# Performance work log

Hardware: AMD Instinct MI355X
Metric: run time of the kernel (lower is better)

## Reference

```python
import jax, jax.numpy as jnp
import numpy as np

N = 8192      # number of WSI patches
DIN = 1024    # input patch-feature dim (dim_in)
DH = 256      # dim_hidden
K = 6         # topk
SCALE = DH ** -0.5

def leaky(x):
    return jax.nn.leaky_relu(x, 0.01)

def setup_inputs() -> dict:
    key = jax.random.key(0)
    ks = jax.random.split(key, 8)
    def w(k, shape, fan_in):
        return jax.random.normal(k, shape, jnp.float32) / np.sqrt(fan_in).astype(np.float32)
    return {
        "x_path": jax.random.normal(ks[0], (N, DIN), jnp.float32),
        "fc1_W": w(ks[1], (DIN, DH), DIN), "fc1_b": jnp.zeros((DH,), jnp.float32),
        "Wh": w(ks[2], (DH, DH), DH), "bh": jnp.zeros((DH,), jnp.float32),
        "Wt": w(ks[3], (DH, DH), DH), "bt": jnp.zeros((DH,), jnp.float32),
        "W1": w(ks[4], (DH, DH), DH), "b1": jnp.zeros((DH,), jnp.float32),
        "W2": w(ks[5], (DH, DH), DH), "b2": jnp.zeros((DH,), jnp.float32),
        "Ag1": w(ks[6], (DH, DH // 2), DH), "bg1": jnp.zeros((DH // 2,), jnp.float32),
        "Ag2": w(ks[7], (DH // 2, 1), DH // 2), "bg2": jnp.zeros((1,), jnp.float32),
    }

def reference(x_path, fc1_W, fc1_b, Wh, bh, Wt, bt, W1, b1, W2, b2, Ag1, bg1, Ag2, bg2):
    # _fc1: Linear(1024->256) + LeakyReLU, then add global mean ("*0.5" mixing)
    x = leaky(x_path @ fc1_W + fc1_b)[None]                 # (1,N,DH)
    x = (x + x.mean(axis=1, keepdims=True)) * 0.5
    e_h = x @ Wh + bh                                        # (1,N,DH)
    e_t = x @ Wt + bt                                        # (1,N,DH)
    # dense attention logits, then top-k neighbor selection
    attn_logit = (e_h * SCALE) @ jnp.swapaxes(e_t, -1, -2)   # (1,N,N)
    topk_w, topk_i = jax.lax.top_k(attn_logit, K)            # (1,N,K)
    p = jax.nn.softmax(topk_w, axis=2)                       # (1,N,K)
    Nb_h = e_t[0][topk_i[0]][None]                           # gather: (1,N,K,DH)
    # message construction
    eh_r = p[..., None] * Nb_h + (1.0 - p)[..., None] * e_h[:, :, None, :]
    gate = jnp.tanh(e_h[:, :, None, :] + eh_r)               # (1,N,K,DH)
    # faithful to torch.einsum('ijkl,ijkm->ijk', Nb_h, gate):
    # l and m are independent -> separable double sum
    ka_w = Nb_h.sum(-1) * gate.sum(-1)                       # (1,N,K)
    ka_p = jax.nn.softmax(ka_w, axis=2)
    e_Nh = jnp.einsum('ink,inkd->ind', ka_p, Nb_h)           # (1,N,DH)
    # message MLPs (dropout in eval mode = identity)
    e_msg = leaky((e_h + e_Nh) @ W1 + b1) + leaky((e_h * e_Nh) @ W2 + b2)
    # GlobalAttention readout: gate_nn = Linear(256,128)+LeakyReLU+Linear(128,1)
    x2 = e_msg[0]                                            # (N,DH)
    g = leaky(x2 @ Ag1 + bg1) @ Ag2 + bg2                    # (N,1)
    g = jax.nn.softmax(g, axis=0)
    e_g = (g * x2).sum(axis=0, keepdims=True)                # (1,DH)
    return e_msg, e_g
```

## Files before the change

### kernel.cpp

```cpp
#include <hip/hip_runtime.h>


typedef __attribute__((ext_vector_type(8))) short short8;
typedef __attribute__((ext_vector_type(4))) short short4v;
typedef __attribute__((ext_vector_type(4))) float f32x4;

__device__ inline float bf2f(unsigned short b) {
    unsigned u = ((unsigned)b) << 16;
    return __builtin_bit_cast(float, u);
}
__device__ inline unsigned short f2bf(float f) {
    unsigned u = __builtin_bit_cast(unsigned, f);
    unsigned r = u + 0x7fffu + ((u >> 16) & 1u);
    return (unsigned short)(r >> 16);
}
__device__ inline f32x4 mfma16(short8 a, short8 b, f32x4 c) {
    return __builtin_amdgcn_mfma_f32_16x16x32_bf16(a, b, c, 0, 0, 0);
}

__device__ inline void gload_lds16(const unsigned short* g, unsigned short* l) {
    __builtin_amdgcn_global_load_lds(
        (const __attribute__((address_space(1))) void*)g,
        (__attribute__((address_space(3))) void*)l, 16, 0, 0);
}

__device__ inline void split8(const f32x4 v0, const f32x4 v1,
                              short8& hi, short8& md, short8& lo) {
    #pragma unroll
    for (int e = 0; e < 8; e++) {
        float a = (e < 4) ? v0[e] : v1[e - 4];
        unsigned ua = __builtin_bit_cast(unsigned, a);
        float h = __builtin_bit_cast(float, ua & 0xFFFF0000u);
        float r1 = a - h;
        unsigned u1 = __builtin_bit_cast(unsigned, r1);
        float m = __builtin_bit_cast(float, u1 & 0xFFFF0000u);
        float r2 = r1 - m;
        unsigned u2 = __builtin_bit_cast(unsigned, r2);
        hi[e] = (short)(ua >> 16);
        md[e] = (short)(u1 >> 16);
        lo[e] = (short)(u2 >> 16);
    }
}
__device__ inline void split4(f32x4 v, short4v& hi, short4v& md, short4v& lo) {
    #pragma unroll
    for (int e = 0; e < 4; e++) {
        float a = v[e];
        unsigned ua = __builtin_bit_cast(unsigned, a);
        float h = __builtin_bit_cast(float, ua & 0xFFFF0000u);
        float r1 = a - h;
        unsigned u1 = __builtin_bit_cast(unsigned, r1);
        float m = __builtin_bit_cast(float, u1 & 0xFFFF0000u);
        float r2 = r1 - m;
        unsigned u2 = __builtin_bit_cast(unsigned, r2);
        hi[e] = (short)(ua >> 16);
        md[e] = (short)(u1 >> 16);
        lo[e] = (short)(u2 >> 16);
    }
}

__device__ inline void tsplit_body(const float* __restrict__ W,
                                   unsigned short* __restrict__ out,
                                   int K, int N, int PS, int bx, int by, int t) {
    __shared__ float T[32][33];
    const int n0 = bx * 32, k0 = by * 32;
    {
        const int r = t >> 3, c = (t & 7) * 4;
        f32x4 v = *(const f32x4*)&W[(size_t)(k0 + r) * N + n0 + c];
        #pragma unroll
        for (int e = 0; e < 4; e++) T[r][c + e] = v[e];
    }
    __syncthreads();
    const int nr = t >> 3, kc = (t & 7) * 4;
    short4v h4, m4, l4;
    #pragma unroll
    for (int e = 0; e < 4; e++) {
        float a = T[kc + e][nr];
        unsigned short h = f2bf(a);
        float r1 = a - bf2f(h);
        unsigned short m = f2bf(r1);
        float r2 = r1 - bf2f(m);
        h4[e] = (short)h; m4[e] = (short)m; l4[e] = (short)f2bf(r2);
    }
    const size_t o = (size_t)(n0 + nr) * K + k0 + kc;
    *(short4v*)&out[o] = h4;
    *(short4v*)&out[(size_t)PS + o] = m4;
    *(short4v*)&out[(size_t)2 * PS + o] = l4;
}
__launch_bounds__(256)
__global__ void tsplit3(const float* __restrict__ W, unsigned short* __restrict__ out,
                        int K, int N, int PS) {
    tsplit_body(W, out, K, N, PS, blockIdx.x, blockIdx.y, threadIdx.x);
}
__launch_bounds__(256)
__global__ void tsplit3p(const float* __restrict__ Wa, const float* __restrict__ Wb,
                         unsigned short* __restrict__ oa, unsigned short* __restrict__ ob,
                         int K, int N, int PS) {
    tsplit_body(blockIdx.z ? Wb : Wa, blockIdx.z ? ob : oa,
                K, N, PS, blockIdx.x, blockIdx.y, threadIdx.x);
}

template <int ASPLIT, int ACT, int ACCUM>
__launch_bounds__(256)
__global__ void gemmM(const void* __restrict__ Av,
                      const unsigned short* __restrict__ Bt,
                      const float* __restrict__ bias, float* __restrict__ C,
                      int N, int K, int BPS) {
    constexpr int APL = ASPLIT ? 3 : 1;
    constexpr int BPL = ASPLIT ? 3 : 2;
    __shared__ __align__(16) unsigned short LA[2][APL * 2048];
    __shared__ __align__(16) unsigned short LB[2][BPL * 2048];
    const int t = threadIdx.x;
    const int r0 = blockIdx.y * 64, c0 = blockIdx.x * 64;
    const int lid = t & 63, w = t >> 6, g = lid >> 4, m16 = lid & 15;
    const int wm = w >> 1, wn = w & 1;

    f32x4 acc[2][2];
    #pragma unroll
    for (int mf = 0; mf < 2; mf++)
        #pragma unroll
        for (int nf = 0; nf < 2; nf++) acc[mf][nf] = {0.0f, 0.0f, 0.0f, 0.0f};

    const int KT = K >> 5;
    const size_t aoff = (size_t)(r0 + (t >> 2)) * K + (t & 3) * 8;
    const size_t boff = (size_t)(c0 + (t >> 2)) * K + (t & 3) * 8;

    {
        #pragma unroll
        for (int p = 0; p < BPL; p++)
            gload_lds16(&Bt[(size_t)p * BPS + boff], &LB[0][p * 2048 + 8 * t]);
        if (ASPLIT) {
            const float* A = (const float*)Av;
            f32x4 v0 = *(const f32x4*)&A[aoff];
            f32x4 v1 = *(const f32x4*)&A[aoff + 4];
            short8 hi, md, lo;
            split8(v0, v1, hi, md, lo);
            *(short8*)&LA[0][8 * t] = hi;
            *(short8*)&LA[0][2048 + 8 * t] = md;
            *(short8*)&LA[0][4096 + 8 * t] = lo;
        } else {
            const unsigned short* A16 = (const unsigned short*)Av;
            gload_lds16(&A16[aoff], &LA[0][8 * t]);
        }
    }
    __syncthreads();

    for (int kt = 0; kt < KT; kt++) {
        const int cur = kt & 1, nxt = cur ^ 1;
        const bool hn = (kt + 1) < KT;
        f32x4 v0, v1;
        if (hn) {
            const size_t ko = (size_t)(kt + 1) * 32;
            #pragma unroll
            for (int p = 0; p < BPL; p++)
                gload_lds16(&Bt[(size_t)p * BPS + boff + ko],
                            &LB[nxt][p * 2048 + 8 * t]);
            if (ASPLIT) {
                const float* A = (const float*)Av;
                v0 = *(const f32x4*)&A[aoff + ko];
                v1 = *(const f32x4*)&A[aoff + ko + 4];
            } else {
                const unsigned short* A16 = (const unsigned short*)Av;
                gload_lds16(&A16[aoff + ko], &LA[nxt][8 * t]);
            }
        }
        short8 af[2][APL], bf[2][BPL];
        #pragma unroll
        for (int mf = 0; mf < 2; mf++) {
            const int row = wm * 32 + mf * 16 + m16;
            #pragma unroll
            for (int p = 0; p < APL; p++)
                af[mf][p] = *(const short8*)&LA[cur][p * 2048 + row * 32 + g * 8];
        }
        #pragma unroll
        for (int nf = 0; nf < 2; nf++) {
            const int col = wn * 32 + nf * 16 + m16;
            #pragma unroll
            for (int p = 0; p < BPL; p++)
                bf[nf][p] = *(const short8*)&LB[cur][p * 2048 + col * 32 + g * 8];
        }
        #pragma unroll
        for (int mf = 0; mf < 2; mf++)
            #pragma unroll
            for (int nf = 0; nf < 2; nf++) {
                if (ASPLIT) {
                    acc[mf][nf] = mfma16(af[mf][0], bf[nf][0], acc[mf][nf]);
                    acc[mf][nf] = mfma16(af[mf][0], bf[nf][1], acc[mf][nf]);
                    acc[mf][nf] = mfma16(af[mf][1], bf[nf][0], acc[mf][nf]);
                    acc[mf][nf] = mfma16(af[mf][0], bf[nf][2], acc[mf][nf]);
                    acc[mf][nf] = mfma16(af[mf][1], bf[nf][1], acc[mf][nf]);
                    acc[mf][nf] = mfma16(af[mf][2], bf[nf][0], acc[mf][nf]);
                } else {
                    acc[mf][nf] = mfma16(af[mf][0], bf[nf][0], acc[mf][nf]);
                    acc[mf][nf] = mfma16(af[mf][0], bf[nf][1], acc[mf][nf]);
                }
            }
        if (hn && ASPLIT) {
            short8 hi, md, lo;
            split8(v0, v1, hi, md, lo);
            *(short8*)&LA[nxt][8 * t] = hi;
            *(short8*)&LA[nxt][2048 + 8 * t] = md;
            *(short8*)&LA[nxt][4096 + 8 * t] = lo;
        }
        __syncthreads();
    }

    #pragma unroll
    for (int nf = 0; nf < 2; nf++) {
        const int col = c0 + wn * 32 + nf * 16 + m16;
        const float bv = bias[col];
        #pragma unroll
        for (int mf = 0; mf < 2; mf++) {
            #pragma unroll
            for (int r = 0; r < 4; r++) {
                const int row = r0 + wm * 32 + mf * 16 + g * 4 + r;
                float v = acc[mf][nf][r] + bv;
                if (ACT == 1) v = v > 0.0f ? v : 0.01f * v;
                size_t idx = (size_t)row * N + col;
                if (ACCUM) v += C[idx];
                C[idx] = v;
            }
        }
    }
}

__launch_bounds__(512)
__global__ void gemmD(const float* __restrict__ A,
                      const unsigned short* __restrict__ BH,
                      const unsigned short* __restrict__ BT,
                      const float* __restrict__ biasH, const float* __restrict__ biasT,
                      float* __restrict__ CH, float* __restrict__ CT, int BPS) {
    __shared__ __align__(16) unsigned short LA[2][3 * 2048];
    __shared__ __align__(16) unsigned short LB[2][6 * 2048];
    const int t = threadIdx.x;
    const int r0 = blockIdx.y * 64, c0 = blockIdx.x * 64;
    const int lid = t & 63, w = t >> 6, g = lid >> 4, m16 = lid & 15;
    const int mat = w >> 2, wsub = w & 3, wm = wsub >> 1, wn = wsub & 1;
    const int K = 256;

    f32x4 acc[2][2];
    #pragma unroll
    for (int mf = 0; mf < 2; mf++)
        #pragma unroll
        for (int nf = 0; nf < 2; nf++) acc[mf][nf] = {0.0f, 0.0f, 0.0f, 0.0f};

    const int arow = t >> 3, akq = (t & 7) * 4;
    const size_t aoff = (size_t)(r0 + arow) * K + akq;
    const int aldst = arow * 32 + akq;
    int bmp[3], bdst[3];
    size_t bsrc[3];
    #pragma unroll
    for (int s = 0; s < 3; s++) {
        int L = t + s * 512;
        int mp = L >> 8;
        bmp[s] = mp;
        bdst[s] = mp * 2048 + (L & 255) * 8;
        int mm = mp >= 3, pl = mp - 3 * mm;
        const unsigned short* base = mm ? BT : BH;
        bsrc[s] = (size_t)(base - BH) + (size_t)pl * BPS +
                  (size_t)(c0 + ((L >> 2) & 63)) * K + (L & 3) * 8;
    }

    {
        #pragma unroll
        for (int s = 0; s < 3; s++)
            gload_lds16(&BH[bsrc[s]], &LB[0][bdst[s]]);
        f32x4 v = *(const f32x4*)&A[aoff];
        #pragma unroll
        for (int e = 0; e < 4; e++) v[e] *= 0.5f;
        short4v hi, md, lo;
        split4(v, hi, md, lo);
        *(short4v*)&LA[0][aldst] = hi;
        *(short4v*)&LA[0][2048 + aldst] = md;
        *(short4v*)&LA[0][4096 + aldst] = lo;
    }
    __syncthreads();

    for (int kt = 0; kt < 8; kt++) {
        const int cur = kt & 1, nxt = cur ^ 1;
        const bool hn = (kt + 1) < 8;
        f32x4 v;
        if (hn) {
            const size_t ko = (size_t)(kt + 1) * 32;
            #pragma unroll
            for (int s = 0; s < 3; s++)
                gload_lds16(&BH[bsrc[s] + ko], &LB[nxt][bdst[s]]);
            v = *(const f32x4*)&A[aoff + ko];
            #pragma unroll
            for (int e = 0; e < 4; e++) v[e] *= 0.5f;
        }
        short8 af[2][3], bf[2][3];
        #pragma unroll
        for (int mf = 0; mf < 2; mf++) {
            const int row = wm * 32 + mf * 16 + m16;
            #pragma unroll
            for (int p = 0; p < 3; p++)
                af[mf][p] = *(const short8*)&LA[cur][p * 2048 + row * 32 + g * 8];
        }
        #pragma unroll
        for (int nf = 0; nf < 2; nf++) {
            const int col = wn * 32 + nf * 16 + m16;
            #pragma unroll
            for (int p = 0; p < 3; p++)
                bf[nf][p] = *(const short8*)
                    &LB[cur][(mat * 3 + p) * 2048 + col * 32 + g * 8];
        }
        #pragma unroll
        for (int mf = 0; mf < 2; mf++)
            #pragma unroll
            for (int nf = 0; nf < 2; nf++) {
                acc[mf][nf] = mfma16(af[mf][0], bf[nf][0], acc[mf][nf]);
                acc[mf][nf] = mfma16(af[mf][0], bf[nf][1], acc[mf][nf]);
                acc[mf][nf] = mfma16(af[mf][1], bf[nf][0], acc[mf][nf]);
                acc[mf][nf] = mfma16(af[mf][0], bf[nf][2], acc[mf][nf]);
                acc[mf][nf] = mfma16(af[mf][1], bf[nf][1], acc[mf][nf]);
                acc[mf][nf] = mfma16(af[mf][2], bf[nf][0], acc[mf][nf]);
            }
        if (hn) {
            short4v hi, md, lo;
            split4(v, hi, md, lo);
            *(short4v*)&LA[nxt][aldst] = hi;
            *(short4v*)&LA[nxt][2048 + aldst] = md;
            *(short4v*)&LA[nxt][4096 + aldst] = lo;
        }
        __syncthreads();
    }

    float* C = mat ? CT : CH;
    const float* bias = mat ? biasT : biasH;
    #pragma unroll
    for (int nf = 0; nf < 2; nf++) {
        const int col = c0 + wn * 32 + nf * 16 + m16;
        const float bv = bias[col];
        #pragma unroll
        for (int mf = 0; mf < 2; mf++) {
            #pragma unroll
            for (int r = 0; r < 4; r++) {
                const int row = r0 + wm * 32 + mf * 16 + g * 4 + r;
                C[(size_t)row * 256 + col] = acc[mf][nf][r] + bv;
            }
        }
    }
}

__launch_bounds__(256)
__global__ void gemmE(const unsigned short* __restrict__ A1,
                      const unsigned short* __restrict__ A2,
                      const unsigned short* __restrict__ P1,
                      const unsigned short* __restrict__ P2,
                      const float* __restrict__ b1, const float* __restrict__ b2,
                      float* __restrict__ C, int BPS) {
    __shared__ __align__(16) unsigned short LA[2][2 * 2048];
    __shared__ __align__(16) unsigned short LB[2][4 * 2048];
    const int t = threadIdx.x;
    const int r0 = blockIdx.y * 64, c0 = blockIdx.x * 64;
    const int lid = t & 63, w = t >> 6, g = lid >> 4, m16 = lid & 15;
    const int wm = w >> 1, wn = w & 1;
    const int K = 256;

    f32x4 acc[2][2][2];
    #pragma unroll
    for (int m = 0; m < 2; m++)
        #pragma unroll
        for (int mf = 0; mf < 2; mf++)
            #pragma unroll
            for (int nf = 0; nf < 2; nf++) acc[m][mf][nf] = {0.0f, 0.0f, 0.0f, 0.0f};

    const size_t aoff = (size_t)(r0 + (t >> 2)) * K + (t & 3) * 8;
    const size_t boff = (size_t)(c0 + (t >> 2)) * K + (t & 3) * 8;

    {
        gload_lds16(&A1[aoff], &LA[0][8 * t]);
        gload_lds16(&A2[aoff], &LA[0][2048 + 8 * t]);
        gload_lds16(&P1[boff], &LB[0][8 * t]);
        gload_lds16(&P1[(size_t)BPS + boff], &LB[0][2048 + 8 * t]);
        gload_lds16(&P2[boff], &LB[0][4096 + 8 * t]);
        gload_lds16(&P2[(size_t)BPS + boff], &LB[0][6144 + 8 * t]);
    }
    __syncthreads();

    for (int kt = 0; kt < 8; kt++) {
        const int cur = kt & 1, nxt = cur ^ 1;
        const bool hn = (kt + 1) < 8;
        if (hn) {
            const size_t ko = (size_t)(kt + 1) * 32;
            gload_lds16(&A1[aoff + ko], &LA[nxt][8 * t]);
            gload_lds16(&A2[aoff + ko], &LA[nxt][2048 + 8 * t]);
            gload_lds16(&P1[boff + ko], &LB[nxt][8 * t]);
            gload_lds16(&P1[(size_t)BPS + boff + ko], &LB[nxt][2048 + 8 * t]);
            gload_lds16(&P2[boff + ko], &LB[nxt][4096 + 8 * t]);
            gload_lds16(&P2[(size_t)BPS + boff + ko], &LB[nxt][6144 + 8 * t]);
        }
        short8 af[2][2], bf[2][2][2];
        #pragma unroll
        for (int m = 0; m < 2; m++)
            #pragma unroll
            for (int mf = 0; mf < 2; mf++) {
                const int row = wm * 32 + mf * 16 + m16;
                af[m][mf] = *(const short8*)&LA[cur][m * 2048 + row * 32 + g * 8];
            }
        #pragma unroll
        for (int m = 0; m < 2; m++)
            #pragma unroll
            for (int nf = 0; nf < 2; nf++) {
                const int col = wn * 32 + nf * 16 + m16;
                #pragma unroll
                for (int p = 0; p < 2; p++)
                    bf[m][nf][p] = *(const short8*)
                        &LB[cur][(m * 2 + p) * 2048 + col * 32 + g * 8];
            }
        #pragma unroll
        for (int m = 0; m < 2; m++)
            #pragma unroll
            for (int mf = 0; mf < 2; mf++)
                #pragma unroll
                for (int nf = 0; nf < 2; nf++) {
                    acc[m][mf][nf] = mfma16(af[m][mf], bf[m][nf][0], acc[m][mf][nf]);
                    acc[m][mf][nf] = mfma16(af[m][mf], bf[m][nf][1], acc[m][mf][nf]);
                }
        __syncthreads();
    }

    #pragma unroll
    for (int nf = 0; nf < 2; nf++) {
        const int col = c0 + wn * 32 + nf * 16 + m16;
        const float bv1 = b1[col], bv2 = b2[col];
        #pragma unroll
        for (int mf = 0; mf < 2; mf++) {
            #pragma unroll
            for (int r = 0; r < 4; r++) {
                const int row = r0 + wm * 32 + mf * 16 + g * 4 + r;
                float v1 = acc[0][mf][nf][r] + bv1;
                v1 = v1 > 0.0f ? v1 : 0.01f * v1;
                float v2 = acc[1][mf][nf][r] + bv2;
                v2 = v2 > 0.0f ? v2 : 0.01f * v2;
                C[(size_t)row * 256 + col] = v1 + v2;
            }
        }
    }
}

__global__ void colsum_k(const float* __restrict__ x, float* __restrict__ out) {
    int d = threadIdx.x, b = blockIdx.x;
    float s = 0.0f;
    int i0 = b * 128;
    for (int i = 0; i < 128; i++) s += x[(size_t)(i0 + i) * 256 + d];
    out[b * 256 + d] = s;
}
__global__ void meanred_k(const float* __restrict__ p, float* __restrict__ mean) {
    int d = threadIdx.x;
    float s = 0.0f;
    for (int b = 0; b < 64; b++) s += p[b * 256 + d];
    mean[d] = s * (1.0f / 8192.0f);
}
__launch_bounds__(256)
__global__ void mwv_k(const float* __restrict__ mean,
                      const float* __restrict__ Wh, const float* __restrict__ bh,
                      const float* __restrict__ Wt, const float* __restrict__ bt,
                      float* __restrict__ biasH, float* __restrict__ biasT) {
    const int n = threadIdx.x;
    const float* W = blockIdx.x ? Wt : Wh;
    const float* bb = blockIdx.x ? bt : bh;
    float* o = blockIdx.x ? biasT : biasH;
    float s = 0.0f;
    for (int d = 0; d < 256; d++) s += mean[d] * W[d * 256 + n];
    o[n] = bb[n] + 0.5f * s;
}
__launch_bounds__(256)
__global__ void prep_k(const float* __restrict__ eh, const float* __restrict__ et,
                       unsigned short* __restrict__ eh16,
                       unsigned short* __restrict__ et16,
                       float* __restrict__ rowsum) {
    const int b = blockIdx.x;
    if (b < 2048) {
        size_t idx = (size_t)b * 256 + threadIdx.x;
        f32x4 v = *(const f32x4*)&eh[idx * 4];
        short4v h;
        #pragma unroll
        for (int e = 0; e < 4; e++) h[e] = (short)f2bf(v[e]);
        *(short4v*)&eh16[idx * 4] = h;
    } else {
        const int w = threadIdx.x >> 6, l = threadIdx.x & 63;
        const int i = (b - 2048) * 4 + w;
        f32x4 v = *(const f32x4*)&et[(size_t)i * 256 + l * 4];
        short4v h;
        #pragma unroll
        for (int e = 0; e < 4; e++) h[e] = (short)f2bf(v[e]);
        *(short4v*)&et16[(size_t)i * 256 + l * 4] = h;
        float s = v[0] + v[1] + v[2] + v[3];
        #pragma unroll
        for (int st = 1; st < 64; st <<= 1) s += __shfl_xor(s, st);
        if (l == 0) rowsum[i] = s;
    }
}

__device__ inline float packkey(float v, unsigned col) {
    unsigned u = (__builtin_bit_cast(unsigned, v) & 0xFFFFF800u) | col;
    return __builtin_bit_cast(float, u);
}
template<int NK>
__device__ inline void insf(float (&tk)[NK], float key) {
    #pragma unroll
    for (int k = 0; k < NK - 1; k++)
        tk[k] = __builtin_amdgcn_fmed3f(key, tk[k + 1], tk[k]);
    tk[NK - 1] = fmaxf(tk[NK - 1], key);
}

__launch_bounds__(512)
__global__ void screen2(const unsigned short* __restrict__ eh16,
                        const unsigned short* __restrict__ et16,
                        int* __restrict__ candi) {
    __shared__ __align__(16) unsigned short Bs[2][2][8192];
    __shared__ float mbuf[8][2][16][8];
    const int t = threadIdx.x;
    const int cs = blockIdx.x;
    const int r0 = blockIdx.y * 128;
    const int w = t >> 6, lid = t & 63, lg = lid >> 4, m16 = lid & 15;
    const int rs = w >> 1, ch = w & 1;

    short8 bfr[2][8];
    #pragma unroll
    for (int s = 0; s < 2; s++)
        #pragma unroll
        for (int ks = 0; ks < 8; ks++)
            bfr[s][ks] = *(const short8*)
                &eh16[(size_t)(r0 + rs * 32 + s * 16 + m16) * 256 + ks * 32 + lg * 8];

    float tk0[6], tk1[6];
    #pragma unroll
    for (int q = 0; q < 6; q++) { tk0[q] = -3.0e38f; tk1[q] = -3.0e38f; }

    int scol[2], goff[2], ldsl[2];
    #pragma unroll
    for (int c = 0; c < 2; c++) {
        int L = (w * 2 + c) * 64 + lid;
        int col = L >> 5, gs = L & 31;
        int gorig = (gs & 24) | ((gs ^ col) & 7);
        scol[c] = col; goff[c] = gorig * 8; ldsl[c] = L * 8;
    }

    #pragma unroll
    for (int tt = 0; tt < 2; tt++) {
        const int j0 = cs * 2048 + tt * 32;
        #pragma unroll
        for (int c = 0; c < 2; c++)
            gload_lds16(&et16[(size_t)(j0 + scol[c]) * 256 + goff[c]],
                        &Bs[0][tt][ldsl[c]]);
    }
    __syncthreads();

    const int swz = m16 & 7;
    const int cbase = (ch * 16 + m16) * 32;
    for (int gi = 0; gi < 32; gi++) {
        const int cur = gi & 1;
        if (gi + 1 < 32) {
            #pragma unroll
            for (int tt = 0; tt < 2; tt++) {
                const int j1 = cs * 2048 + ((gi + 1) * 2 + tt) * 32;
                #pragma unroll
                for (int c = 0; c < 2; c++)
                    gload_lds16(&et16[(size_t)(j1 + scol[c]) * 256 + goff[c]],
                                &Bs[cur ^ 1][tt][ldsl[c]]);
            }
        }
        #pragma unroll
        for (int tt = 0; tt < 2; tt++) {
            const int tile = gi * 2 + tt;
            const unsigned short* bst = Bs[cur][tt];
            f32x4 a0 = {0.0f, 0.0f, 0.0f, 0.0f}, a1 = a0;
            #pragma unroll
            for (int ks = 0; ks < 8; ks++) {
                const int gq = ks * 4 + lg;
                short8 e = *(const short8*)&bst[(cbase + (gq ^ swz)) * 8];
                a0 = mfma16(e, bfr[0][ks], a0);
                a1 = mfma16(e, bfr[1][ks], a1);
            }
            const unsigned cb = (unsigned)(tile * 32 + ch * 16 + lg * 4);
            #pragma unroll
            for (int r = 0; r < 4; r++) {
                insf<6>(tk0, packkey(a0[r], cb + (unsigned)r));
                insf<6>(tk1, packkey(a1[r], cb + (unsigned)r));
            }
        }
        __syncthreads();
    }

    #pragma unroll
    for (int s = 0; s < 2; s++) {
        float tk8[8];
        tk8[0] = -3.0e38f; tk8[1] = -3.0e38f;
        #pragma unroll
        for (int q = 0; q < 6; q++) tk8[q + 2] = s ? tk1[q] : tk0[q];
        #pragma unroll
        for (int step = 16; step <= 32; step <<= 1) {
            float ok[8];
            #pragma unroll
            for (int q = 0; q < 8; q++) ok[q] = __shfl_xor(tk8[q], step);
            #pragma unroll
            for (int q = 0; q < 8; q++) insf<8>(tk8, ok[q]);
        }
        if (lg == 0) {
            #pragma unroll
            for (int q = 0; q < 8; q++) mbuf[rs * 2 + s][ch][m16][q] = tk8[q];
        }
    }
    __syncthreads();

    if (t < 128) {
        float tk8[8];
        #pragma unroll
        for (int q = 0; q < 8; q++) tk8[q] = mbuf[t >> 4][0][t & 15][q];
        #pragma unroll
        for (int q = 0; q < 8; q++) insf<8>(tk8, mbuf[t >> 4][1][t & 15][q]);
        const int row = r0 + t;
        #pragma unroll
        for (int q = 0; q < 8; q++)
            candi[(size_t)row * 32 + cs * 8 + q] =
                cs * 2048 + (int)(__builtin_bit_cast(unsigned, tk8[q]) & 0x7FFu);
    }
}

__launch_bounds__(256)
__global__ void stageD(const float* __restrict__ eh, const float* __restrict__ et,
                       const float* __restrict__ rowsum,
                       const int* __restrict__ candi,
                       unsigned short* __restrict__ m1, unsigned short* __restrict__ m2) {
    const int w = threadIdx.x >> 6, l = threadIdx.x & 63;
    const int i = blockIdx.x * 4 + w;
    const int c_own = l & 31;

    const int jown = candi[(size_t)i * 32 + c_own] & 8191;

    const int q = l & 7, g8 = l >> 3;
    const float* er = &eh[(size_t)i * 256];
    double vres[4];
    #pragma unroll
    for (int p = 0; p < 4; p++) {
        const int cc = p * 8 + g8;
        const int jc = __shfl(jown, cc);
        const float* tr = &et[(size_t)jc * 256];
        double a = 0.0;
        #pragma unroll
        for (int tt = 0; tt < 8; tt++) {
            const int o = (tt * 8 + q) * 4;
            f32x4 av = *(const f32x4*)&er[o];
            f32x4 bv = *(const f32x4*)&tr[o];
            a += (double)av[0] * bv[0] + (double)av[1] * bv[1] +
                 (double)av[2] * bv[2] + (double)av[3] * bv[3];
        }
        a += __shfl_xor(a, 1);
        a += __shfl_xor(a, 2);
        a += __shfl_xor(a, 4);
        vres[p] = a * 0.0625;
    }
    const int src = (c_own & 7) * 8;
    double t0 = __shfl(vres[0], src), t1 = __shfl(vres[1], src);
    double t2 = __shfl(vres[2], src), t3 = __shfl(vres[3], src);
    const int ps = c_own >> 3;
    double v = ps == 0 ? t0 : ps == 1 ? t1 : ps == 2 ? t2 : t3;

    unsigned long long kb = __builtin_bit_cast(unsigned long long, v);
    double key = __builtin_bit_cast(double, (kb & ~31ULL) | (unsigned long long)c_own);
    float wf[6]; int selc[6];
    #pragma unroll
    for (int s = 0; s < 6; s++) {
        double b = key;
        #pragma unroll
        for (int st = 1; st < 32; st <<= 1) {
            double ob = __shfl_xor(b, st);
            b = b > ob ? b : ob;
        }
        selc[s] = (int)(__builtin_bit_cast(unsigned long long, b) & 31ULL);
        wf[s] = (float)b;
        if (key == b) key = -1.0e300;
    }
    int selj[6];
    #pragma unroll
    for (int s = 0; s < 6; s++) selj[s] = __shfl(jown, selc[s]);

    float sp[6];
    {
        float mx = wf[0];
        #pragma unroll
        for (int s = 1; s < 6; s++) mx = fmaxf(mx, wf[s]);
        float se = 0.0f, e6[6];
        #pragma unroll
        for (int s = 0; s < 6; s++) { e6[s] = expf(wf[s] - mx); se += e6[s]; }
        #pragma unroll
        for (int s = 0; s < 6; s++) sp[s] = e6[s] / se;
    }

    f32x4 eh4 = *(const f32x4*)&eh[(size_t)i * 256 + l * 4];
    f32x4 nb[6];
    #pragma unroll
    for (int k = 0; k < 6; k++)
        nb[k] = *(const f32x4*)&et[(size_t)selj[k] * 256 + l * 4];

    float pgs[6], pns[6];
    #pragma unroll
    for (int k = 0; k < 6; k++) {
        const float pk = sp[k];
        float pg = 0.0f;
        #pragma unroll
        for (int e = 0; e < 4; e++) {
            float ehd = eh4[e], nbd = nb[k][e];
            float ehr = pk * nbd + (1.0f - pk) * ehd;
            pg += tanhf(ehd + ehr);
        }
        #pragma unroll
        for (int st = 1; st < 64; st <<= 1) pg += __shfl_xor(pg, st);
        pgs[k] = pg;
        pns[k] = rowsum[selj[k]];
    }

    float skp[6];
    {
        float ka[6], mx = -3.0e38f, se = 0.0f;
        #pragma unroll
        for (int k = 0; k < 6; k++) { ka[k] = pns[k] * pgs[k]; mx = fmaxf(mx, ka[k]); }
        #pragma unroll
        for (int k = 0; k < 6; k++) { ka[k] = expf(ka[k] - mx); se += ka[k]; }
        #pragma unroll
        for (int k = 0; k < 6; k++) skp[k] = ka[k] / se;
    }

    f32x4 enh = {0.0f, 0.0f, 0.0f, 0.0f};
    #pragma unroll
    for (int k = 0; k < 6; k++) {
        const float kp = skp[k];
        #pragma unroll
        for (int e = 0; e < 4; e++) enh[e] += kp * nb[k][e];
    }
    short4v h1, h2;
    #pragma unroll
    for (int e = 0; e < 4; e++) {
        h1[e] = (short)f2bf(eh4[e] + enh[e]);
        h2[e] = (short)f2bf(eh4[e] * enh[e]);
    }
    *(short4v*)&m1[(size_t)i * 256 + l * 4] = h1;
    *(short4v*)&m2[(size_t)i * 256 + l * 4] = h2;
}

__launch_bounds__(256)
__global__ void gate2_k(const float* __restrict__ g1, const float* __restrict__ Ag2,
                        const float* __restrict__ bg2, float* __restrict__ glog) {
    const int i = blockIdx.x * 256 + threadIdx.x;
    float s = 0.0f;
    #pragma unroll 4
    for (int h = 0; h < 128; h++) s += g1[(size_t)i * 128 + h] * Ag2[h];
    glog[i] = s + bg2[0];
}

__launch_bounds__(1024)
__global__ void softmax_g(const float* __restrict__ glog, float* __restrict__ gexp,
                          float* __restrict__ scal) {
    const int t = threadIdx.x;
    __shared__ float red[1024];
    float v[8];
    float m = -3.0e38f;
    #pragma unroll
    for (int c = 0; c < 8; c++) { v[c] = glog[t + c * 1024]; m = fmaxf(m, v[c]); }
    red[t] = m; __syncthreads();
    for (int st = 512; st > 0; st >>= 1) {
        if (t < st) red[t] = fmaxf(red[t], red[t + st]);
        __syncthreads();
    }
    float gm = red[0]; __syncthreads();
    float s = 0.0f;
    #pragma unroll
    for (int c = 0; c < 8; c++) {
        float e = expf(v[c] - gm);
        gexp[t + c * 1024] = e;
        s += e;
    }
    red[t] = s; __syncthreads();
    for (int st = 512; st > 0; st >>= 1) {
        if (t < st) red[t] += red[t + st];
        __syncthreads();
    }
    if (t == 0) scal[0] = 1.0f / red[0];
}

__launch_bounds__(256)
__global__ void wsum_k(const float* __restrict__ emsg, const float* __restrict__ gexp,
                       float* __restrict__ egp) {
    const int b = blockIdx.x, d = threadIdx.x;
    float s = 0.0f;
    const int i0 = b * 128;
    for (int i = 0; i < 128; i++) s += gexp[i0 + i] * emsg[(size_t)(i0 + i) * 256 + d];
    egp[b * 256 + d] = s;
}
__global__ void egfinal_f(const float* __restrict__ egp, const float* __restrict__ scal,
                          float* __restrict__ out) {
    const int d = threadIdx.x;
    float s = 0.0f;
    for (int b = 0; b < 64; b++) s += egp[b * 256 + d];
    out[d] = s * scal[0];
}

__global__ void wsbad_k(float* __restrict__ out) { out[3] = 9000.0f; }

extern "C" void kernel_launch(void* const* d_in, const int* in_sizes, int n_in,
                              void* d_out, int out_size, void* d_ws, size_t ws_size,
                              hipStream_t stream) {
    (void)in_sizes; (void)n_in; (void)out_size;
    const float* x_path = (const float*)d_in[0];
    const float* fc1_W  = (const float*)d_in[1];
    const float* fc1_b  = (const float*)d_in[2];
    const float* Wh     = (const float*)d_in[3];
    const float* bh     = (const float*)d_in[4];
    const float* Wt     = (const float*)d_in[5];
    const float* bt     = (const float*)d_in[6];
    const float* W1     = (const float*)d_in[7];
    const float* b1     = (const float*)d_in[8];
    const float* W2     = (const float*)d_in[9];
    const float* b2     = (const float*)d_in[10];
    const float* Ag1    = (const float*)d_in[11];
    const float* bg1    = (const float*)d_in[12];
    const float* Ag2    = (const float*)d_in[13];
    const float* bg2    = (const float*)d_in[14];
    float* out_f = (float*)d_out;

    const size_t WS_NEEDED = 26412048;
    if (ws_size < WS_NEEDED) {
        hipLaunchKernelGGL(wsbad_k, dim3(1), dim3(1), 0, stream, out_f);
        return;
    }

    char* ws = (char*)d_ws;
    float* x     = (float*)(ws + 0);
    unsigned short* eh16 = (unsigned short*)(ws + 0);
    unsigned short* et16 = (unsigned short*)(ws + 4194304);
    unsigned short* m1b  = (unsigned short*)(ws + 0);
    unsigned short* m2b  = (unsigned short*)(ws + 4194304);
    float* g1    = (float*)(ws + 0);
    float* eh    = (float*)(ws + 8388608);
    float* emsg  = out_f;
    float* et    = (float*)(ws + 16777216);
    int*   candi = (int*)  (ws + 25165824);
    float* rowsum= (float*)(ws + 26214400);
    float* meanp = (float*)(ws + 26214400);
    float* biasH = (float*)(ws + 26247168);
    float* biasT = (float*)(ws + 26248192);
    float* meanv = (float*)(ws + 26279936);
    float* glog  = (float*)(ws + 26280960);
    float* gexp  = (float*)(ws + 26313728);
    float* egp   = (float*)(ws + 26346496);
    float* scal  = (float*)(ws + 26412032);

    unsigned short* Fp = (unsigned short*)(ws + 16777216);
    unsigned short* WHp = (unsigned short*)(ws + 25165824);
    unsigned short* WTp = (unsigned short*)(ws + 25559040);
    unsigned short* P1 = (unsigned short*)(ws + 16777216);
    unsigned short* P2 = (unsigned short*)(ws + 17170432);
    unsigned short* Gp = (unsigned short*)(ws + 25165824);

    dim3 gg(4, 128);
    hipLaunchKernelGGL(tsplit3, dim3(8, 32), dim3(256), 0, stream,
                       fc1_W, Fp, 1024, 256, 262144);
    hipLaunchKernelGGL((gemmM<1, 1, 0>), gg, dim3(256), 0, stream,
                       (const void*)x_path, Fp, fc1_b, x, 256, 1024, 262144);
    hipLaunchKernelGGL(colsum_k, dim3(64), dim3(256), 0, stream, x, meanp);
    hipLaunchKernelGGL(meanred_k, dim3(1), dim3(256), 0, stream, meanp, meanv);
    hipLaunchKernelGGL(tsplit3p, dim3(8, 8, 2), dim3(256), 0, stream,
                       Wh, Wt, WHp, WTp, 256, 256, 65536);
    hipLaunchKernelGGL(mwv_k, dim3(2), dim3(256), 0, stream,
                       meanv, Wh, bh, Wt, bt, biasH, biasT);
    hipLaunchKernelGGL(gemmD, gg, dim3(512), 0, stream,
                       x, WHp, WTp, biasH, biasT, eh, et, 65536);
    hipLaunchKernelGGL(prep_k, dim3(4096), dim3(256), 0, stream,
                       eh, et, eh16, et16, rowsum);
    hipLaunchKernelGGL(screen2, dim3(4, 64), dim3(512), 0, stream, eh16, et16, candi);
    hipLaunchKernelGGL(stageD, dim3(2048), dim3(256), 0, stream, eh, et, rowsum,
                       candi, m1b, m2b);
    hipLaunchKernelGGL(tsplit3p, dim3(8, 8, 2), dim3(256), 0, stream,
                       W1, W2, P1, P2, 256, 256, 65536);
    hipLaunchKernelGGL(gemmE, gg, dim3(256), 0, stream,
                       m1b, m2b, P1, P2, b1, b2, emsg, 65536);
    hipLaunchKernelGGL(tsplit3, dim3(4, 8), dim3(256), 0, stream,
                       Ag1, Gp, 256, 128, 32768);
    hipLaunchKernelGGL((gemmM<1, 1, 0>), dim3(2, 128), dim3(256), 0, stream,
                       (const void*)emsg, Gp, bg1, g1, 128, 256, 32768);
    hipLaunchKernelGGL(gate2_k, dim3(32), dim3(256), 0, stream, g1, Ag2, bg2, glog);
    hipLaunchKernelGGL(softmax_g, dim3(1), dim3(1024), 0, stream, glog, gexp, scal);
    hipLaunchKernelGGL(wsum_k, dim3(64), dim3(256), 0, stream, emsg, gexp, egp);
    hipLaunchKernelGGL(egfinal_f, dim3(1), dim3(256), 0, stream, egp, scal, out_f + 2097152);
}
```

Measured before the change: 312.0 us.

## Fuse weight-split launches, mean reduction, bf16 prep and gate projection into neighbours

Merges the separate weight-split launches into two multi-matrix kernels and folds the mean reduction into the bias kernel. The bf16 conversion of e_h now happens inside the screening kernel, so the prep pass only handles e_t. The second gate layer (dot with Ag2) moves into a new GEMM epilogue that reduces by shuffles and accumulates into glog with atomics; glog is zeroed in colsum. This removes several launches and the g1 round trip through memory, at the cost of nondeterministic atomic summation order. bg2 is dropped, which is safe because softmax is shift-invariant.

```diff
diff --git a/kernel.cpp b/kernel.cpp
--- a/kernel.cpp
+++ b/kernel.cpp
@@ -87,16 +87,26 @@
     *(short4v*)&out[(size_t)2 * PS + o] = l4;
 }
 __launch_bounds__(256)
-__global__ void tsplit3(const float* __restrict__ W, unsigned short* __restrict__ out,
-                        int K, int N, int PS) {
-    tsplit_body(W, out, K, N, PS, blockIdx.x, blockIdx.y, threadIdx.x);
+__global__ void tsplitAll(const float* __restrict__ fc1_W, const float* __restrict__ Wh,
+                          const float* __restrict__ Wt,
+                          unsigned short* __restrict__ Fp,
+                          unsigned short* __restrict__ WHp,
+                          unsigned short* __restrict__ WTp) {
+    const int idx = blockIdx.x, t = threadIdx.x;
+    if (idx < 256) tsplit_body(fc1_W, Fp, 1024, 256, 262144, idx & 7, idx >> 3, t);
+    else if (idx < 320) { int r = idx - 256; tsplit_body(Wh, WHp, 256, 256, 65536, r & 7, r >> 3, t); }
+    else { int r = idx - 320; tsplit_body(Wt, WTp, 256, 256, 65536, r & 7, r >> 3, t); }
 }
 __launch_bounds__(256)
-__global__ void tsplit3p(const float* __restrict__ Wa, const float* __restrict__ Wb,
-                         unsigned short* __restrict__ oa, unsigned short* __restrict__ ob,
-                         int K, int N, int PS) {
-    tsplit_body(blockIdx.z ? Wb : Wa, blockIdx.z ? ob : oa,
-                K, N, PS, blockIdx.x, blockIdx.y, threadIdx.x);
+__global__ void tsplit3t(const float* __restrict__ W1, const float* __restrict__ W2,
+                         const float* __restrict__ Ag1,
+                         unsigned short* __restrict__ P1,
+                         unsigned short* __restrict__ P2,
+                         unsigned short* __restrict__ Gp) {
+    const int idx = blockIdx.x, t = threadIdx.x;
+    if (idx < 64) tsplit_body(W1, P1, 256, 256, 65536, idx & 7, idx >> 3, t);
+    else if (idx < 128) { int r = idx - 64; tsplit_body(W2, P2, 256, 256, 65536, r & 7, r >> 3, t); }
+    else { int r = idx - 128; tsplit_body(Ag1, Gp, 256, 128, 32768, r & 3, r >> 2, t); }
 }
 
 template <int ASPLIT, int ACT, int ACCUM>
@@ -246,13 +256,12 @@
     const int arow = t >> 3, akq = (t & 7) * 4;
     const size_t aoff = (size_t)(r0 + arow) * K + akq;
     const int aldst = arow * 32 + akq;
-    int bmp[3], bdst[3];
+    int bdst[3];
     size_t bsrc[3];
     #pragma unroll
     for (int s = 0; s < 3; s++) {
         int L = t + s * 512;
         int mp = L >> 8;
-        bmp[s] = mp;
         bdst[s] = mp * 2048 + (L & 255) * 8;
         int mm = mp >= 3, pl = mp - 3 * mm;
         const unsigned short* base = mm ? BT : BH;
@@ -439,25 +448,149 @@
     }
 }
 
-__global__ void colsum_k(const float* __restrict__ x, float* __restrict__ out) {
+__launch_bounds__(256)
+__global__ void gemmG(const float* __restrict__ A,
+                      const unsigned short* __restrict__ Bt,
+                      const float* __restrict__ bias,
+                      const float* __restrict__ Ag2, float* __restrict__ glog,
+                      int BPS) {
+    __shared__ __align__(16) unsigned short LA[2][3 * 2048];
+    __shared__ __align__(16) unsigned short LB[2][3 * 2048];
+    const int t = threadIdx.x;
+    const int r0 = blockIdx.y * 64, c0 = blockIdx.x * 64;
+    const int lid = t & 63, w = t >> 6, g = lid >> 4, m16 = lid & 15;
+    const int wm = w >> 1, wn = w & 1;
+    const int K = 256;
+
+    f32x4 acc[2][2];
+    #pragma unroll
+    for (int mf = 0; mf < 2; mf++)
+        #pragma unroll
+        for (int nf = 0; nf < 2; nf++) acc[mf][nf] = {0.0f, 0.0f, 0.0f, 0.0f};
+
+    const size_t aoff = (size_t)(r0 + (t >> 2)) * K + (t & 3) * 8;
+    const size_t boff = (size_t)(c0 + (t >> 2)) * K + (t & 3) * 8;
+
+    {
+        #pragma unroll
+        for (int p = 0; p < 3; p++)
+            gload_lds16(&Bt[(size_t)p * BPS + boff], &LB[0][p * 2048 + 8 * t]);
+        f32x4 v0 = *(const f32x4*)&A[aoff];
+        f32x4 v1 = *(const f32x4*)&A[aoff + 4];
+        short8 hi, md, lo;
+        split8(v0, v1, hi, md, lo);
+        *(short8*)&LA[0][8 * t] = hi;
+        *(short8*)&LA[0][2048 + 8 * t] = md;
+        *(short8*)&LA[0][4096 + 8 * t] = lo;
+    }
+    __syncthreads();
+
+    for (int kt = 0; kt < 8; kt++) {
+        const int cur = kt & 1, nxt = cur ^ 1;
+        const bool hn = (kt + 1) < 8;
+        f32x4 v0, v1;
+        if (hn) {
+            const size_t ko = (size_t)(kt + 1) * 32;
+            #pragma unroll
+            for (int p = 0; p < 3; p++)
+                gload_lds16(&Bt[(size_t)p * BPS + boff + ko],
+                            &LB[nxt][p * 2048 + 8 * t]);
+            v0 = *(const f32x4*)&A[aoff + ko];
+            v1 = *(const f32x4*)&A[aoff + ko + 4];
+        }
+        short8 af[2][3], bf[2][3];
+        #pragma unroll
+        for (int mf = 0; mf < 2; mf++) {
+            const int row = wm * 32 + mf * 16 + m16;
+            #pragma unroll
+            for (int p = 0; p < 3; p++)
+                af[mf][p] = *(const short8*)&LA[cur][p * 2048 + row * 32 + g * 8];
+        }
+        #pragma unroll
+        for (int nf = 0; nf < 2; nf++) {
+            const int col = wn * 32 + nf * 16 + m16;
+            #pragma unroll
+            for (int p = 0; p < 3; p++)
+                bf[nf][p] = *(const short8*)&LB[cur][p * 2048 + col * 32 + g * 8];
+        }
+        #pragma unroll
+        for (int mf = 0; mf < 2; mf++)
+            #pragma unroll
+            for (int nf = 0; nf < 2; nf++) {
+                acc[mf][nf] = mfma16(af[mf][0], bf[nf][0], acc[mf][nf]);
+                acc[mf][nf] = mfma16(af[mf][0], bf[nf][1], acc[mf][nf]);
+                acc[mf][nf] = mfma16(af[mf][1], bf[nf][0], acc[mf][nf]);
+                acc[mf][nf] = mfma16(af[mf][0], bf[nf][2], acc[mf][nf]);
+                acc[mf][nf] = mfma16(af[mf][1], bf[nf][1], acc[mf][nf]);
+                acc[mf][nf] = mfma16(af[mf][2], bf[nf][0], acc[mf][nf]);
+            }
+        if (hn) {
+            short8 hi, md, lo;
+            split8(v0, v1, hi, md, lo);
+            *(short8*)&LA[nxt][8 * t] = hi;
+            *(short8*)&LA[nxt][2048 + 8 * t] = md;
+            *(short8*)&LA[nxt][4096 + 8 * t] = lo;
+        }
+        __syncthreads();
+    }
+
+    float pp[2][4];
+    #pragma unroll
+    for (int mf = 0; mf < 2; mf++)
+        #pragma unroll
+        for (int r = 0; r < 4; r++) pp[mf][r] = 0.0f;
+    #pragma unroll
+    for (int nf = 0; nf < 2; nf++) {
+        const int col = c0 + wn * 32 + nf * 16 + m16;
+        const float bv = bias[col], a2 = Ag2[col];
+        #pragma unroll
+        for (int mf = 0; mf < 2; mf++) {
+            #pragma unroll
+            for (int r = 0; r < 4; r++) {
+                float v = acc[mf][nf][r] + bv;
+                v = v > 0.0f ? v : 0.01f * v;
+                pp[mf][r] += v * a2;
+            }
+        }
+    }
+    #pragma unroll
+    for (int st = 1; st < 16; st <<= 1)
+        #pragma unroll
+        for (int mf = 0; mf < 2; mf++)
+            #pragma unroll
+            for (int r = 0; r < 4; r++) pp[mf][r] += __shfl_xor(pp[mf][r], st);
+    if (m16 == 0) {
+        #pragma unroll
+        for (int mf = 0; mf < 2; mf++)
+            #pragma unroll
+            for (int r = 0; r < 4; r++)
+                atomicAdd(&glog[r0 + wm * 32 + mf * 16 + g * 4 + r], pp[mf][r]);
+    }
+}
+
+__global__ void colsum_k(const float* __restrict__ x, float* __restrict__ out,
+                         float* __restrict__ glog) {
     int d = threadIdx.x, b = blockIdx.x;
     float s = 0.0f;
     int i0 = b * 128;
     for (int i = 0; i < 128; i++) s += x[(size_t)(i0 + i) * 256 + d];
     out[b * 256 + d] = s;
-}
-__global__ void meanred_k(const float* __restrict__ p, float* __restrict__ mean) {
-    int d = threadIdx.x;
-    float s = 0.0f;
-    for (int b = 0; b < 64; b++) s += p[b * 256 + d];
-    mean[d] = s * (1.0f / 8192.0f);
+    int tid = b * 256 + d;
+    if (tid < 8192) glog[tid] = 0.0f;
 }
 __launch_bounds__(256)
-__global__ void mwv_k(const float* __restrict__ mean,
+__global__ void mwv_k(const float* __restrict__ meanp,
                       const float* __restrict__ Wh, const float* __restrict__ bh,
                       const float* __restrict__ Wt, const float* __restrict__ bt,
                       float* __restrict__ biasH, float* __restrict__ biasT) {
+    __shared__ float mean[256];
     const int n = threadIdx.x;
+    {
+        float s = 0.0f;
+        for (int b = 0; b < 64; b++) s += meanp[b * 256 + n];
+        mean[n] = s * (1.0f / 8192.0f);
+    }
+    __syncthreads();
     const float* W = blockIdx.x ? Wt : Wh;
     const float* bb = blockIdx.x ? bt : bh;
     float* o = blockIdx.x ? biasT : biasH;
@@ -466,31 +599,19 @@
     o[n] = bb[n] + 0.5f * s;
 }
 __launch_bounds__(256)
-__global__ void prep_k(const float* __restrict__ eh, const float* __restrict__ et,
-                       unsigned short* __restrict__ eh16,
-                       unsigned short* __restrict__ et16,
-                       float* __restrict__ rowsum) {
-    const int b = blockIdx.x;
-    if (b < 2048) {
-        size_t idx = (size_t)b * 256 + threadIdx.x;
-        f32x4 v = *(const f32x4*)&eh[idx * 4];
-        short4v h;
-        #pragma unroll
-        for (int e = 0; e < 4; e++) h[e] = (short)f2bf(v[e]);
-        *(short4v*)&eh16[idx * 4] = h;
-    } else {
-        const int w = threadIdx.x >> 6, l = threadIdx.x & 63;
-        const int i = (b - 2048) * 4 + w;
-        f32x4 v = *(const f32x4*)&et[(size_t)i * 256 + l * 4];
-        short4v h;
-        #pragma unroll
-        for (int e = 0; e < 4; e++) h[e] = (short)f2bf(v[e]);
-        *(short4v*)&et16[(size_t)i * 256 + l * 4] = h;
-        float s = v[0] + v[1] + v[2] + v[3];
-        #pragma unroll
-        for (int st = 1; st < 64; st <<= 1) s += __shfl_xor(s, st);
-        if (l == 0) rowsum[i] = s;
-    }
+__global__ void epk(const float* __restrict__ et, unsigned short* __restrict__ et16,
+                    float* __restrict__ rowsum) {
+    const int w = threadIdx.x >> 6, l = threadIdx.x & 63;
+    const int i = blockIdx.x * 4 + w;
+    f32x4 v = *(const f32x4*)&et[(size_t)i * 256 + l * 4];
+    short4v h;
+    #pragma unroll
+    for (int e = 0; e < 4; e++) h[e] = (short)f2bf(v[e]);
+    *(short4v*)&et16[(size_t)i * 256 + l * 4] = h;
+    float s = v[0] + v[1] + v[2] + v[3];
+    #pragma unroll
+    for (int st = 1; st < 64; st <<= 1) s += __shfl_xor(s, st);
+    if (l == 0) rowsum[i] = s;
 }
 
 __device__ inline float packkey(float v, unsigned col) {
@@ -506,7 +627,7 @@
 }
 
 __launch_bounds__(512)
-__global__ void screen2(const unsigned short* __restrict__ eh16,
+__global__ void screen2(const float* __restrict__ eh,
                         const unsigned short* __restrict__ et16,
                         int* __restrict__ candi) {
     __shared__ __align__(16) unsigned short Bs[2][2][8192];
@@ -521,9 +642,19 @@
     #pragma unroll
     for (int s = 0; s < 2; s++)
         #pragma unroll
-        for (int ks = 0; ks < 8; ks++)
-            bfr[s][ks] = *(const short8*)
-                &eh16[(size_t)(r0 + rs * 32 + s * 16 + m16) * 256 + ks * 32 + lg * 8];
+        for (int ks = 0; ks < 8; ks++) {
+            const float* p = &eh[(size_t)(r0 + rs * 32 + s * 16 + m16) * 256
+                                 + ks * 32 + lg * 8];
+            f32x4 a = *(const f32x4*)p;
+            f32x4 b = *(const f32x4*)(p + 4);
+            short8 hh;
+            #pragma unroll
+            for (int e = 0; e < 4; e++) {
+                hh[e] = (short)f2bf(a[e]);
+                hh[4 + e] = (short)f2bf(b[e]);
+            }
+            bfr[s][ks] = hh;
+        }
 
     float tk0[6], tk1[6];
     #pragma unroll
@@ -738,16 +869,6 @@
     }
     *(short4v*)&m1[(size_t)i * 256 + l * 4] = h1;
     *(short4v*)&m2[(size_t)i * 256 + l * 4] = h2;
-}
-
-__launch_bounds__(256)
-__global__ void gate2_k(const float* __restrict__ g1, const float* __restrict__ Ag2,
-                        const float* __restrict__ bg2, float* __restrict__ glog) {
-    const int i = blockIdx.x * 256 + threadIdx.x;
-    float s = 0.0f;
-    #pragma unroll 4
-    for (int h = 0; h < 128; h++) s += g1[(size_t)i * 128 + h] * Ag2[h];
-    glog[i] = s + bg2[0];
 }
 
 __launch_bounds__(1024)
@@ -817,7 +938,6 @@
     const float* Ag1    = (const float*)d_in[11];
     const float* bg1    = (const float*)d_in[12];
     const float* Ag2    = (const float*)d_in[13];
-    const float* bg2    = (const float*)d_in[14];
     float* out_f = (float*)d_out;
 
     const size_t WS_NEEDED = 26412048;
@@ -828,11 +948,9 @@
 
     char* ws = (char*)d_ws;
     float* x     = (float*)(ws + 0);
-    unsigned short* eh16 = (unsigned short*)(ws + 0);
     unsigned short* et16 = (unsigned short*)(ws + 4194304);
     unsigned short* m1b  = (unsigned short*)(ws + 0);
     unsigned short* m2b  = (unsigned short*)(ws + 4194304);
-    float* g1    = (float*)(ws + 0);
     float* eh    = (float*)(ws + 8388608);
     float* emsg  = out_f;
     float* et    = (float*)(ws + 16777216);
@@ -841,7 +959,6 @@
     float* meanp = (float*)(ws + 26214400);
     float* biasH = (float*)(ws + 26247168);
     float* biasT = (float*)(ws + 26248192);
-    float* meanv = (float*)(ws + 26279936);
     float* glog  = (float*)(ws + 26280960);
     float* gexp  = (float*)(ws + 26313728);
     float* egp   = (float*)(ws + 26346496);
@@ -855,32 +972,25 @@
     unsigned short* Gp = (unsigned short*)(ws + 25165824);
 
     dim3 gg(4, 128);
-    hipLaunchKernelGGL(tsplit3, dim3(8, 32), dim3(256), 0, stream,
-                       fc1_W, Fp, 1024, 256, 262144);
+    hipLaunchKernelGGL(tsplitAll, dim3(384), dim3(256), 0, stream,
+                       fc1_W, Wh, Wt, Fp, WHp, WTp);
     hipLaunchKernelGGL((gemmM<1, 1, 0>), gg, dim3(256), 0, stream,
                        (const void*)x_path, Fp, fc1_b, x, 256, 1024, 262144);
-    hipLaunchKernelGGL(colsum_k, dim3(64), dim3(256), 0, stream, x, meanp);
-    hipLaunchKernelGGL(meanred_k, dim3(1), dim3(256), 0, stream, meanp, meanv);
-    hipLaunchKernelGGL(tsplit3p, dim3(8, 8, 2), dim3(256), 0, stream,
-                       Wh, Wt, WHp, WTp, 256, 256, 65536);
+    hipLaunchKernelGGL(colsum_k, dim3(64), dim3(256), 0, stream, x, meanp, glog);
     hipLaunchKernelGGL(mwv_k, dim3(2), dim3(256), 0, stream,
-                       meanv, Wh, bh, Wt, bt, biasH, biasT);
+                       meanp, Wh, bh, Wt, bt, biasH, biasT);
     hipLaunchKernelGGL(gemmD, gg, dim3(512), 0, stream,
                        x, WHp, WTp, biasH, biasT, eh, et, 65536);
-    hipLaunchKernelGGL(prep_k, dim3(4096), dim3(256), 0, stream,
-                       eh, et, eh16, et16, rowsum);
-    hipLaunchKernelGGL(screen2, dim3(4, 64), dim3(512), 0, stream, eh16, et16, candi);
+    hipLaunchKernelGGL(epk, dim3(2048), dim3(256), 0, stream, et, et16, rowsum);
+    hipLaunchKernelGGL(screen2, dim3(4, 64), dim3(512), 0, stream, eh, et16, candi);
     hipLaunchKernelGGL(stageD, dim3(2048), dim3(256), 0, stream, eh, et, rowsum,
                        candi, m1b, m2b);
-    hipLaunchKernelGGL(tsplit3p, dim3(8, 8, 2), dim3(256), 0, stream,
-                       W1, W2, P1, P2, 256, 256, 65536);
+    hipLaunchKernelGGL(tsplit3t, dim3(160), dim3(256), 0, stream,
+                       W1, W2, Ag1, P1, P2, Gp);
     hipLaunchKernelGGL(gemmE, gg, dim3(256), 0, stream,
                        m1b, m2b, P1, P2, b1, b2, emsg, 65536);
-    hipLaunchKernelGGL(tsplit3, dim3(4, 8), dim3(256), 0, stream,
-                       Ag1, Gp, 256, 128, 32768);
-    hipLaunchKernelGGL((gemmM<1, 1, 0>), dim3(2, 128), dim3(256), 0, stream,
-                       (const void*)emsg, Gp, bg1, g1, 128, 256, 32768);
-    hipLaunchKernelGGL(gate2_k, dim3(32), dim3(256), 0, stream, g1, Ag2, bg2, glog);
+    hipLaunchKernelGGL(gemmG, dim3(2, 128), dim3(256), 0, stream,
+                       emsg, Gp, bg1, Ag2, glog, 32768);
     hipLaunchKernelGGL(softmax_g, dim3(1), dim3(1024), 0, stream, glog, gexp, scal);
     hipLaunchKernelGGL(wsum_k, dim3(64), dim3(256), 0, stream, emsg, gexp, egp);
     hipLaunchKernelGGL(egfinal_f, dim3(1), dim3(256), 0, stream, egp, scal, out_f + 2097152);
```

Result: faster. 300.5 us (-3.7%).
